# Optimization experiments

Hardware: AMD Instinct MI355X
Metric: run time of the kernel (lower is better)

Reference implementation:

```python
import jax, jax.numpy as jnp
import numpy as np

N = 50000          # nodes per side (variables == clauses here)
IN, HID, OUT = 64, 128, 128
H = 4              # attention heads (self and cross)
P = 2              # num_meta_paths
E = 640000         # edges per graph
NEG = 0.2          # leaky_relu negative slope


def _glorot(key, shape):
    fan = shape[-2] + shape[-1]
    return (jax.random.normal(key, shape) * jnp.sqrt(2.0 / fan)).astype(jnp.float32)


def _ln(x, g, b):
    mu = x.mean(-1, keepdims=True)
    v = ((x - mu) ** 2).mean(-1, keepdims=True)
    return (x - mu) / jnp.sqrt(v + 1e-5) * g + b


def _segment_softmax(s, seg, num):
    # s: [E, H]; softmax over edges sharing the same seg id
    smax = jax.ops.segment_max(s, seg, num_segments=num)
    e = jnp.exp(s - smax[seg])
    den = jax.ops.segment_sum(e, seg, num_segments=num)
    return e / (den[seg] + 1e-16)


def _agg(alpha, feats, src, dst, num):
    # out[d, h, c] = sum_{e: dst[e]=d} alpha[e,h] * feats[src[e], c]
    gathered = feats[src]  # [E, C]
    outs = [jax.ops.segment_sum(alpha[:, h:h + 1] * gathered, dst, num_segments=num)
            for h in range(alpha.shape[1])]
    return jnp.stack(outs, axis=1)  # [num, H, C]


def _hga_self(x, adj, W, att_l, att_r, bias):
    # homogeneous HGAConv with self loops, concat=False (mean over heads)
    n = x.shape[0]
    xl = x @ W.T                      # [N, C]
    al = xl @ att_l                   # [N, H]
    ar = xl @ att_r                   # [N, H]
    loops = jnp.arange(n)
    src = jnp.concatenate([adj[0], loops])
    dst = jnp.concatenate([adj[1], loops])
    score = al[dst] + ar[src]         # edge_score: a_l[adj[1]] + a_r[adj[0]]
    alpha = _segment_softmax(jax.nn.leaky_relu(score, NEG), dst, n)
    out = _agg(alpha, xl, src, dst, n).mean(axis=1)  # [N, C]
    return out + bias


def _hga_cross(xv, xc, adj, Wl, Wr, att_l, att_r, bias):
    # bipartite HGAConv: adj[1] indexes var nodes, adj[0] indexes cls nodes
    n, m = xv.shape[0], xc.shape[0]
    xl = xv @ Wl.T
    xr = xc @ Wr.T
    al = xl @ att_l
    ar = xr @ att_r
    ar_ = xl @ att_r
    al_ = xr @ att_l
    c_idx, v_idx = adj[0], adj[1]
    score = al[v_idx] + ar[c_idx]        # -> normalized per var node
    score_ = ar_[v_idx] + al_[c_idx]     # transposed direction -> per cls node
    alpha = _segment_softmax(jax.nn.leaky_relu(score, NEG), v_idx, n)
    alpha_ = _segment_softmax(jax.nn.leaky_relu(score_, NEG), c_idx, m)
    out_var = _agg(alpha, xr, c_idx, v_idx, n).mean(axis=1) + bias   # [n, OUT]
    out_cls = _agg(alpha_, xl, v_idx, c_idx, m).mean(axis=1) + bias  # [m, OUT]
    return out_var, out_cls


def setup_inputs() -> dict:
    key = jax.random.key(0)
    ks = jax.random.split(key, 32)
    d = {}
    d['x_var'] = jax.random.normal(ks[0], (N, IN), dtype=jnp.float32)
    d['x_cls'] = jax.random.normal(ks[1], (N, IN), dtype=jnp.float32)
    d['mp_var'] = jax.random.randint(ks[2], (P, 2, E), 0, N)
    d['mp_cls'] = jax.random.randint(ks[3], (P, 2, E), 0, N)
    d['adj_pos'] = jax.random.randint(ks[4], (2, E), 0, N)
    d['adj_neg'] = jax.random.randint(ks[5], (2, E), 0, N)
    d['W_var_emb'] = _glorot(ks[6], (HID, IN))
    d['W_cls_emb'] = _glorot(ks[7], (HID, IN))
    d['ln_var_g'] = jnp.ones(HID); d['ln_var_b'] = jnp.zeros(HID)
    d['ln_cls_g'] = jnp.ones(HID); d['ln_cls_b'] = jnp.zeros(HID)
    d['var_pw'] = jnp.ones(P); d['cls_pw'] = jnp.ones(P)
    d['sv_W'] = _glorot(ks[8], (P, HID, HID))
    d['sv_al'] = _glorot(ks[9], (P, HID, H))
    d['sv_ar'] = _glorot(ks[10], (P, HID, H))
    d['sv_b'] = jnp.zeros((P, HID))
    d['sc_W'] = _glorot(ks[11], (P, HID, HID))
    d['sc_al'] = _glorot(ks[12], (P, HID, H))
    d['sc_ar'] = _glorot(ks[13], (P, HID, H))
    d['sc_b'] = jnp.zeros((P, HID))
    d['cp_Wl'] = _glorot(ks[14], (OUT, HID))
    d['cp_Wr'] = _glorot(ks[15], (OUT, HID))
    d['cp_al'] = _glorot(ks[16], (OUT, H))
    d['cp_ar'] = _glorot(ks[17], (OUT, H))
    d['cp_b'] = jnp.zeros(OUT)
    d['cn_Wl'] = _glorot(ks[18], (OUT, HID))
    d['cn_Wr'] = _glorot(ks[19], (OUT, HID))
    d['cn_al'] = _glorot(ks[20], (OUT, H))
    d['cn_ar'] = _glorot(ks[21], (OUT, H))
    d['cn_b'] = jnp.zeros(OUT)
    return d


def reference(x_var, x_cls, mp_var, mp_cls, adj_pos, adj_neg,
              W_var_emb, W_cls_emb, ln_var_g, ln_var_b, ln_cls_g, ln_cls_b,
              var_pw, cls_pw, sv_W, sv_al, sv_ar, sv_b, sc_W, sc_al, sc_ar, sc_b,
              cp_Wl, cp_Wr, cp_al, cp_ar, cp_b, cn_Wl, cn_Wr, cn_al, cn_ar, cn_b):
    xv = x_var @ W_var_emb.T          # [N, HID]
    xc = x_cls @ W_cls_emb.T
    # pre-norm residual self-attention, weighted sum over meta paths
    hv = _ln(xv, ln_var_g, ln_var_b)
    hc = _ln(xc, ln_cls_g, ln_cls_b)
    av = sum(var_pw[p] * _hga_self(hv, mp_var[p], sv_W[p], sv_al[p], sv_ar[p], sv_b[p]) for p in range(P))
    ac = sum(cls_pw[p] * _hga_self(hc, mp_cls[p], sc_W[p], sc_al[p], sc_ar[p], sc_b[p]) for p in range(P))
    xv = xv + av
    xc = xc + ac
    # bipartite cross attention over positive / negative literal edges
    vpos, cpos = _hga_cross(xv, xc, adj_pos, cp_Wl, cp_Wr, cp_al, cp_ar, cp_b)
    vneg, cneg = _hga_cross(xv, xc, adj_neg, cn_Wl, cn_Wr, cn_al, cn_ar, cn_b)
    return jnp.stack([vpos + vneg, cpos + cneg])  # [2, N, OUT]
```

## Files before the change

### kernel.cpp

```cpp
#include <hip/hip_runtime.h>
#include <hip/hip_bf16.h>

#define NN 50000
#define EE 640000
#define NEG 0.2f
#define CAP 64

#define BSH 9
#define NBKT 98
#define FCAP 7168
#define CHUNKA 8192
#define PA_B 79

struct Ptr8 { const int* p[8]; };
struct MArgs { const float* w[8]; const float* al[8]; const float* ar[8]; };

struct SegArg {
    const int* starts;
    const int* counts;
    const unsigned short* srt;
    const float* adst;
    const float* asrc;
    const unsigned short* feats;
    const float* pw;
    int pwi;
    int hasLoop;
};

typedef __attribute__((ext_vector_type(8))) short short8;
typedef __attribute__((ext_vector_type(8))) unsigned short ushort8;
typedef __attribute__((ext_vector_type(4))) float floatx4;

__device__ __forceinline__ unsigned short f2bf(float x) {
    unsigned b = __float_as_uint(x);
    b = b + 0x7fffu + ((b >> 16) & 1u);
    return (unsigned short)(b >> 16);
}

__device__ __forceinline__ float4 leakyexp4(float4 ad, float4 as) {
    float v0 = ad.x + as.x, v1 = ad.y + as.y, v2 = ad.z + as.z, v3 = ad.w + as.w;
    v0 = v0 > 0.f ? v0 : NEG * v0;
    v1 = v1 > 0.f ? v1 : NEG * v1;
    v2 = v2 > 0.f ? v2 : NEG * v2;
    v3 = v3 > 0.f ? v3 : NEG * v3;
    return make_float4(__expf(v0), __expf(v1), __expf(v2), __expf(v3));
}

__global__ void transpose_emb(const float* __restrict__ wev, const float* __restrict__ wec,
                              float* __restrict__ out)
{
    int i = blockIdx.x * 256 + threadIdx.x;
    if (i < 8192) { out[i] = wev[(i & 127) * 64 + (i >> 7)]; return; }
    if (i < 16384) { int j = i - 8192; out[i] = wec[(j & 127) * 64 + (j >> 7)]; }
}

__global__ void make_M(MArgs a, float* __restrict__ Mbuf)
{
    int b = blockIdx.x;
    const float* W  = a.w[b];
    const float* AL = a.al[b];
    const float* AR = a.ar[b];
    for (int e = threadIdx.x; e < 1024; e += 256) {
        int k = e >> 3, h = e & 7;
        const float* att = (h < 4) ? AL : AR;
        int hh = h & 3;
        float s = 0.f;
        for (int c = 0; c < 128; c++) s += W[c * 128 + k] * att[c * 4 + hh];
        Mbuf[b * 1024 + e] = s;
    }
}

__global__ void embed_ln(const float* __restrict__ x, const float* __restrict__ Wt,
                         const float* __restrict__ g, const float* __restrict__ b,
                         const float* __restrict__ pw, const float* __restrict__ sb,
                         float* __restrict__ F, float* __restrict__ C)
{
    __shared__ float lx[8][64];
    __shared__ float red[2][8][2];
    int c = threadIdx.x;
    int n0 = blockIdx.x * 8;
    for (int t = c; t < 8 * 64; t += 128) {
        lx[t >> 6][t & 63] = x[(size_t)(n0 + (t >> 6)) * 64 + (t & 63)];
    }
    __syncthreads();
    float acc[8];
#pragma unroll
    for (int m = 0; m < 8; m++) acc[m] = 0.f;
    for (int k = 0; k < 64; k++) {
        float w = Wt[k * 128 + c];
#pragma unroll
        for (int m = 0; m < 8; m++) acc[m] += lx[m][k] * w;
    }
    int lane = c & 63, wv = c >> 6;
#pragma unroll
    for (int m = 0; m < 8; m++) {
        float s1 = acc[m], s2 = acc[m] * acc[m];
        for (int off = 32; off; off >>= 1) { s1 += __shfl_xor(s1, off); s2 += __shfl_xor(s2, off); }
        if (lane == 0) { red[wv][m][0] = s1; red[wv][m][1] = s2; }
    }
    __syncthreads();
    float biassum = pw[0] * sb[c] + pw[1] * sb[128 + c];
    float gg = g[c], bb = b[c];
#pragma unroll
    for (int m = 0; m < 8; m++) {
        float s1 = red[0][m][0] + red[1][m][0];
        float s2 = red[0][m][1] + red[1][m][1];
        float mu  = s1 * (1.f / 128.f);
        float var = s2 * (1.f / 128.f) - mu * mu;
        float inv = rsqrtf(var + 1e-5f);
        float v = acc[m];
        size_t idx = (size_t)(n0 + m) * 128 + c;
        F[idx] = v + biassum;
        C[idx] = (v - mu) * inv * gg + bb;
    }
}

__device__ __forceinline__ void stage_W(const float* __restrict__ W,
                                        unsigned short* __restrict__ WL, int t)
{
    for (int i = t; i < 2048; i += 256) {
        int n = i >> 4, c16 = i & 15;
        const float* src = W + n * 128 + c16 * 8;
        short8 v;
#pragma unroll
        for (int j = 0; j < 8; j++) v[j] = (short)f2bf(src[j]);
        *(short8*)&WL[(n * 16 + (c16 ^ (n & 15))) * 8] = v;
    }
}

__global__ __launch_bounds__(256) void mfma_proj2(
    const float* __restrict__ in,
    const float* __restrict__ W0, const float* __restrict__ W1,
    const float* __restrict__ M0, const float* __restrict__ M1,
    unsigned short* __restrict__ ob0, unsigned short* __restrict__ ob1,
    float4* __restrict__ dl0, float4* __restrict__ dr0,
    float4* __restrict__ dl1, float4* __restrict__ dr1)
{
    __shared__ unsigned short WL[16384];
    __shared__ float ML[2048];

    int t = threadIdx.x;
    stage_W(W0, WL, t);
    for (int i = t; i < 1024; i += 256) { ML[i] = M0[i]; ML[1024 + i] = M1[i]; }
    __syncthreads();

    int w = t >> 6, lane = t & 63;
    int ln = lane & 15, quad = lane >> 4;
    int rbase = blockIdx.x * 64 + w * 16;
    int row = rbase + ln;
    int arow = (row < NN) ? row : (NN - 1);

    short8 afrag[4];
    float p[16];
#pragma unroll
    for (int h = 0; h < 16; h++) p[h] = 0.f;
#pragma unroll
    for (int kc = 0; kc < 4; kc++) {
        int k0 = kc * 32 + quad * 8;
        const float* ap = in + (size_t)arow * 128 + k0;
        float av[8];
#pragma unroll
        for (int j = 0; j < 8; j++) av[j] = ap[j];
#pragma unroll
        for (int j = 0; j < 8; j++) {
            afrag[kc][j] = (short)f2bf(av[j]);
            const float* m0 = &ML[(k0 + j) * 8];
            const float* m1 = &ML[1024 + (k0 + j) * 8];
#pragma unroll
            for (int h = 0; h < 8; h++) { p[h] += av[j] * m0[h]; p[8 + h] += av[j] * m1[h]; }
        }
    }
#pragma unroll
    for (int h = 0; h < 16; h++) {
        p[h] += __shfl_xor(p[h], 16);
        p[h] += __shfl_xor(p[h], 32);
    }
    if (quad == 0 && row < NN) {
        dl0[row] = make_float4(p[0], p[1], p[2], p[3]);
        dr0[row] = make_float4(p[4], p[5], p[6], p[7]);
        dl1[row] = make_float4(p[8], p[9], p[10], p[11]);
        dr1[row] = make_float4(p[12], p[13], p[14], p[15]);
    }

#pragma unroll
    for (int ct = 0; ct < 8; ct++) {
        floatx4 acc = {0.f, 0.f, 0.f, 0.f};
#pragma unroll
        for (int kc = 0; kc < 4; kc++) {
            int c16 = kc * 4 + quad;
            int n = ct * 16 + ln;
            short8 bfr = *(const short8*)&WL[(n * 16 + (c16 ^ ln)) * 8];
            acc = __builtin_amdgcn_mfma_f32_16x16x32_bf16(afrag[kc], bfr, acc, 0, 0, 0);
        }
#pragma unroll
        for (int r = 0; r < 4; r++) {
            int rr = rbase + quad * 4 + r;
            if (rr < NN) ob0[(size_t)rr * 128 + ct * 16 + ln] = f2bf(acc[r]);
        }
    }
    __syncthreads();
    stage_W(W1, WL, t);
    __syncthreads();
#pragma unroll
    for (int ct = 0; ct < 8; ct++) {
        floatx4 acc = {0.f, 0.f, 0.f, 0.f};
#pragma unroll
        for (int kc = 0; kc < 4; kc++) {
            int c16 = kc * 4 + quad;
            int n = ct * 16 + ln;
            short8 bfr = *(const short8*)&WL[(n * 16 + (c16 ^ ln)) * 8];
            acc = __builtin_amdgcn_mfma_f32_16x16x32_bf16(afrag[kc], bfr, acc, 0, 0, 0);
        }
#pragma unroll
        for (int r = 0; r < 4; r++) {
            int rr = rbase + quad * 4 + r;
            if (rr < NN) ob1[(size_t)rr * 128 + ct * 16 + ln] = f2bf(acc[r]);
        }
    }
}

__global__ void zero_bcnt(int* __restrict__ p)
{
    int i = blockIdx.x * 256 + threadIdx.x;
    if (i < 8 * NBKT) p[i] = 0;
}

__global__ void bucket_count(Ptr8 dst, int* __restrict__ bcnt)
{
    __shared__ int h[NBKT];
    int l = blockIdx.x / PA_B, cb = blockIdx.x % PA_B;
    const int* dp = dst.p[l];
    for (int i = threadIdx.x; i < NBKT; i += 256) h[i] = 0;
    __syncthreads();
    int e0 = cb * CHUNKA;
    for (int i = threadIdx.x; i < CHUNKA; i += 256) {
        int e = e0 + i;
        if (e < EE) atomicAdd(&h[dp[e] >> BSH], 1);
    }
    __syncthreads();
    for (int i = threadIdx.x; i < NBKT; i += 256)
        if (h[i]) atomicAdd(&bcnt[l * NBKT + i], h[i]);
}

__global__ void bucket_scan(const int* __restrict__ bcnt, int* __restrict__ bstart,
                            int* __restrict__ bcur)
{
    __shared__ int sh[NBKT];
    int l = blockIdx.x;
    for (int i = threadIdx.x; i < NBKT; i += 256) sh[i] = bcnt[l * NBKT + i];
    __syncthreads();
    if (threadIdx.x == 0) {
        int acc = 0;
        for (int i = 0; i < NBKT; i++) { int t = sh[i]; sh[i] = acc; acc += t; }
    }
    __syncthreads();
    for (int i = threadIdx.x; i < NBKT; i += 256) {
        bstart[l * (NBKT + 1) + i] = sh[i];
        bcur[l * NBKT + i] = sh[i];
    }
    if (threadIdx.x == 0) bstart[l * (NBKT + 1) + NBKT] = EE;
}

__global__ void bucket_place(Ptr8 src, Ptr8 dst, int* __restrict__ bcur,
                             unsigned* __restrict__ recs)
{
    __shared__ int h[NBKT];
    __shared__ int base[NBKT];
    int l = blockIdx.x / PA_B, cb = blockIdx.x % PA_B;
    const int* sp = src.p[l];
    const int* dp = dst.p[l];
    for (int i = threadIdx.x; i < NBKT; i += 256) h[i] = 0;
    __syncthreads();
    int e0 = cb * CHUNKA;
    for (int i = threadIdx.x; i < CHUNKA; i += 256) {
        int e = e0 + i;
        if (e < EE) atomicAdd(&h[dp[e] >> BSH], 1);
    }
    __syncthreads();
    for (int i = threadIdx.x; i < NBKT; i += 256) {
        int c = h[i];
        base[i] = c ? atomicAdd(&bcur[l * NBKT + i], c) : 0;
        h[i] = 0;
    }
    __syncthreads();
    unsigned* rl = recs + (size_t)l * EE;
    for (int i = threadIdx.x; i < CHUNKA; i += 256) {
        int e = e0 + i;
        if (e >= EE) continue;
        int d = dp[e];
        int b = d >> BSH;
        int pos = base[b] + atomicAdd(&h[b], 1);
        rl[pos] = ((unsigned)sp[e] << 16) | (unsigned)d;
    }
}

__global__ __launch_bounds__(256) void bucket_final(
    const unsigned* __restrict__ recs, const int* __restrict__ bstart,
    int* __restrict__ starts8, int* __restrict__ counts8,
    unsigned short* __restrict__ sortedU)
{
    __shared__ unsigned R[FCAP];
    __shared__ int cnt[512];
    __shared__ int cur[512];
    __shared__ int psum[256];
    int l = blockIdx.x / NBKT, b = blockIdx.x % NBKT;
    int d0 = b << BSH;
    int nd = min(512, NN - d0);
    int ebase = bstart[l * (NBKT + 1) + b];
    int ecnt  = bstart[l * (NBKT + 1) + b + 1] - ebase;
    const unsigned* rp = recs + (size_t)l * EE + ebase;
    int t = threadIdx.x;
    bool inLds = (ecnt <= FCAP);

    for (int i = t; i < 512; i += 256) cnt[i] = 0;
    __syncthreads();
    for (int i = t; i < ecnt; i += 256) {
        unsigned r = rp[i];
        if (inLds) R[i] = r;
        atomicAdd(&cnt[(r & 0xffffu) - d0], 1);
    }
    __syncthreads();
    int s0 = cnt[2 * t] + cnt[2 * t + 1];
    psum[t] = s0;
    __syncthreads();
    for (int off = 1; off < 256; off <<= 1) {
        int x = (t >= off) ? psum[t - off] : 0;
        __syncthreads();
        psum[t] += x;
        __syncthreads();
    }
    int excl = psum[t] - s0;
    cur[2 * t] = excl;
    cur[2 * t + 1] = excl + cnt[2 * t];
    __syncthreads();
    for (int i = t; i < nd; i += 256) {
        starts8[l * NN + d0 + i] = ebase + cur[i];
        counts8[l * NN + d0 + i] = cnt[i];
    }
    __syncthreads();
    unsigned short* so = sortedU + (size_t)l * EE + ebase;
    for (int i = t; i < ecnt; i += 256) {
        unsigned r = inLds ? R[i] : rp[i];
        int dloc = (int)(r & 0xffffu) - d0;
        int pos = atomicAdd(&cur[dloc], 1);
        so[pos] = (unsigned short)(r >> 16);
    }
}

__global__ __launch_bounds__(256, 8) void agg_fused(
    SegArg A, SegArg B,
    const float* __restrict__ bias0, const float* __restrict__ bias1,
    float* __restrict__ acc, int mode)
{
    __shared__ float          wSh[16][CAP];
    __shared__ unsigned short sSh[16][CAP];

    int t = threadIdx.x;
    int gid = t >> 4;
    int sub = t & 15;
    int seg = gid & 1;
    int d   = blockIdx.x * 8 + (gid >> 1);

    const int* starts = seg ? B.starts : A.starts;
    const int* counts = seg ? B.counts : A.counts;
    const unsigned short* srt = seg ? B.srt : A.srt;
    const float* adst = seg ? B.adst : A.adst;
    const float* asrc = seg ? B.asrc : A.asrc;
    const unsigned short* feats = seg ? B.feats : A.feats;
    const float* pw = seg ? B.pw : A.pw;
    int pwi = seg ? B.pwi : A.pwi;
    int hasLoop = seg ? B.hasLoop : A.hasLoop;

    int base = starts[d];
    int k = counts[d];
    int kTot = k + hasLoop;

    float4 ad = *(const float4*)(adst + (size_t)d * 4);

    float p0 = 0.f, p1 = 0.f, p2 = 0.f, p3 = 0.f;
    for (int i = sub; i < kTot; i += 16) {
        int s = (i < k) ? (int)srt[base + i] : d;
        if (i < CAP) sSh[gid][i] = (unsigned short)s;
        float4 as = *(const float4*)(asrc + (size_t)s * 4);
        float4 e = leakyexp4(ad, as);
        p0 += e.x; p1 += e.y; p2 += e.z; p3 += e.w;
    }
#pragma unroll
    for (int off = 1; off <= 8; off <<= 1) {
        p0 += __shfl_xor(p0, off); p1 += __shfl_xor(p1, off);
        p2 += __shfl_xor(p2, off); p3 += __shfl_xor(p3, off);
    }
    float scale = 0.25f * (pw ? pw[pwi] : 1.0f);
    float i0 = scale / (p0 + 1e-16f);
    float i1 = scale / (p1 + 1e-16f);
    float i2 = scale / (p2 + 1e-16f);
    float i3 = scale / (p3 + 1e-16f);

    int kW = kTot < CAP ? kTot : CAP;
    for (int i = sub; i < kW; i += 16) {
        int s = (int)sSh[gid][i];
        float4 as = *(const float4*)(asrc + (size_t)s * 4);
        float4 e = leakyexp4(ad, as);
        wSh[gid][i] = e.x * i0 + e.y * i1 + e.z * i2 + e.w * i3;
    }

    float a[8];
#pragma unroll
    for (int i = 0; i < 8; i++) a[i] = 0.f;
    const unsigned short* fbase = feats + sub * 8;
    for (int j = 0; j < kW; ++j) {
        float wgt = wSh[gid][j];
        int s = (int)sSh[gid][j];
        ushort8 v = *(const ushort8*)(fbase + (size_t)s * 128);
#pragma unroll
        for (int i = 0; i < 8; i++)
            a[i] += wgt * __uint_as_float((unsigned)(unsigned short)v[i] << 16);
    }
    for (int j = CAP; j < kTot; ++j) {
        int s = (j < k) ? (int)srt[base + j] : d;
        float4 as = *(const float4*)(asrc + (size_t)s * 4);
        float4 e = leakyexp4(ad, as);
        float wgt = e.x * i0 + e.y * i1 + e.z * i2 + e.w * i3;
        ushort8 v = *(const ushort8*)(fbase + (size_t)s * 128);
#pragma unroll
        for (int i = 0; i < 8; i++)
            a[i] += wgt * __uint_as_float((unsigned)(unsigned short)v[i] << 16);
    }

#pragma unroll
    for (int i = 0; i < 8; i++) a[i] += __shfl_xor(a[i], 16);

    if (seg == 0) {
        size_t idx = (size_t)d * 128 + sub * 8;
        float4* ap = (float4*)(acc + idx);
        float4 lo = make_float4(a[0], a[1], a[2], a[3]);
        float4 hi = make_float4(a[4], a[5], a[6], a[7]);
        if (mode) {
            const float4* b0 = (const float4*)(bias0 + sub * 8);
            const float4* b1 = (const float4*)(bias1 + sub * 8);
            float4 c0 = b0[0], c1 = b0[1], d0v = b1[0], d1v = b1[1];
            ap[0] = make_float4(c0.x + d0v.x + lo.x, c0.y + d0v.y + lo.y,
                                c0.z + d0v.z + lo.z, c0.w + d0v.w + lo.w);
            ap[1] = make_float4(c1.x + d1v.x + hi.x, c1.y + d1v.y + hi.y,
                                c1.z + d1v.z + hi.z, c1.w + d1v.w + hi.w);
        } else {
            float4 r0 = ap[0], r1 = ap[1];
            ap[0] = make_float4(r0.x + lo.x, r0.y + lo.y, r0.z + lo.z, r0.w + lo.w);
            ap[1] = make_float4(r1.x + hi.x, r1.y + hi.y, r1.z + hi.z, r1.w + hi.w);
        }
    }
}

extern "C" void kernel_launch(void* const* d_in, const int* in_sizes, int n_in,
                              void* d_out, int out_size, void* d_ws, size_t ws_size,
                              hipStream_t stream)
{
    const float* x_var   = (const float*)d_in[0];
    const float* x_cls   = (const float*)d_in[1];
    const int*   mp_var  = (const int*)d_in[2];
    const int*   mp_cls  = (const int*)d_in[3];
    const int*   adj_pos = (const int*)d_in[4];
    const int*   adj_neg = (const int*)d_in[5];
    const float* W_var_emb = (const float*)d_in[6];
    const float* W_cls_emb = (const float*)d_in[7];
    const float* ln_var_g = (const float*)d_in[8];
    const float* ln_var_b = (const float*)d_in[9];
    const float* ln_cls_g = (const float*)d_in[10];
    const float* ln_cls_b = (const float*)d_in[11];
    const float* var_pw = (const float*)d_in[12];
    const float* cls_pw = (const float*)d_in[13];
    const float* sv_W  = (const float*)d_in[14];
    const float* sv_al = (const float*)d_in[15];
    const float* sv_ar = (const float*)d_in[16];
    const float* sv_b  = (const float*)d_in[17];
    const float* sc_W  = (const float*)d_in[18];
    const float* sc_al = (const float*)d_in[19];
    const float* sc_ar = (const float*)d_in[20];
    const float* sc_b  = (const float*)d_in[21];
    const float* cp_Wl = (const float*)d_in[22];
    const float* cp_Wr = (const float*)d_in[23];
    const float* cp_al = (const float*)d_in[24];
    const float* cp_ar = (const float*)d_in[25];
    const float* cp_b  = (const float*)d_in[26];
    const float* cn_Wl = (const float*)d_in[27];
    const float* cn_Wr = (const float*)d_in[28];
    const float* cn_al = (const float*)d_in[29];
    const float* cn_ar = (const float*)d_in[30];
    const float* cn_b  = (const float*)d_in[31];

    float* out0 = (float*)d_out;
    float* out1 = out0 + (size_t)NN * 128;

    float* ws = (float*)d_ws;
    size_t off = 0;
    auto alloc = [&](size_t n) { float* p = ws + off; off += n; return p; };
    float* Wt   = alloc(16384);
    float* Mbuf = alloc(8 * 1024);
    float* F   = alloc((size_t)NN * 128);
    float* G   = alloc((size_t)NN * 128);
    float* C   = alloc((size_t)NN * 128);
    float* D   = alloc((size_t)NN * 128);
    unsigned short* B1 = (unsigned short*)alloc((size_t)NN * 64);
    unsigned short* B2 = (unsigned short*)alloc((size_t)NN * 64);
    float* dl   = alloc(NN * 4);
    float* dr   = alloc(NN * 4);
    float* dl2  = alloc(NN * 4);
    float* dr2  = alloc(NN * 4);
    float* dl3  = alloc(NN * 4);
    float* dr3  = alloc(NN * 4);
    float* dl4  = alloc(NN * 4);
    float* dr4  = alloc(NN * 4);
    int* counts8 = (int*)alloc(8 * NN);
    int* starts8 = (int*)alloc(8 * NN);
    int* bcnt    = (int*)alloc(8 * NBKT);
    int* bstart  = (int*)alloc(8 * (NBKT + 1));
    int* bcur    = (int*)alloc(8 * NBKT);
    unsigned* recs = (unsigned*)alloc((size_t)8 * EE);
    unsigned short* sortedU = (unsigned short*)alloc((size_t)4 * EE);

    unsigned short* Pc = (unsigned short*)C;
    unsigned short* Pd = (unsigned short*)C + (size_t)NN * 128;

    const float* WtEv = Wt;
    const float* WtEc = Wt + 8192;

    Ptr8 srcP, dstP;
    srcP.p[0] = mp_var;            dstP.p[0] = mp_var + EE;
    srcP.p[1] = mp_var + 2 * EE;   dstP.p[1] = mp_var + 3 * EE;
    srcP.p[2] = mp_cls;            dstP.p[2] = mp_cls + EE;
    srcP.p[3] = mp_cls + 2 * EE;   dstP.p[3] = mp_cls + 3 * EE;
    srcP.p[4] = adj_pos;           dstP.p[4] = adj_pos + EE;
    srcP.p[5] = adj_pos + EE;      dstP.p[5] = adj_pos;
    srcP.p[6] = adj_neg;           dstP.p[6] = adj_neg + EE;
    srcP.p[7] = adj_neg + EE;      dstP.p[7] = adj_neg;

    MArgs ma;
    ma.w[0] = sv_W;           ma.al[0] = sv_al;        ma.ar[0] = sv_ar;
    ma.w[1] = sv_W + 16384;   ma.al[1] = sv_al + 512;  ma.ar[1] = sv_ar + 512;
    ma.w[2] = sc_W;           ma.al[2] = sc_al;        ma.ar[2] = sc_ar;
    ma.w[3] = sc_W + 16384;   ma.al[3] = sc_al + 512;  ma.ar[3] = sc_ar + 512;
    ma.w[4] = cp_Wl;          ma.al[4] = cp_al;        ma.ar[4] = cp_ar;
    ma.w[5] = cp_Wr;          ma.al[5] = cp_al;        ma.ar[5] = cp_ar;
    ma.w[6] = cn_Wl;          ma.al[6] = cn_al;        ma.ar[6] = cn_ar;
    ma.w[7] = cn_Wr;          ma.al[7] = cn_al;        ma.ar[7] = cn_ar;

    zero_bcnt<<<(8 * NBKT + 255) / 256, 256, 0, stream>>>(bcnt);
    bucket_count<<<8 * PA_B, 256, 0, stream>>>(dstP, bcnt);
    bucket_scan<<<8, 256, 0, stream>>>(bcnt, bstart, bcur);
    bucket_place<<<8 * PA_B, 256, 0, stream>>>(srcP, dstP, bcur, recs);
    bucket_final<<<8 * NBKT, 256, 0, stream>>>(recs, bstart, starts8, counts8, sortedU);

    transpose_emb<<<64, 256, 0, stream>>>(W_var_emb, W_cls_emb, Wt);
    make_M<<<8, 256, 0, stream>>>(ma, Mbuf);
    embed_ln<<<NN / 8, 128, 0, stream>>>(x_var, WtEv, ln_var_g, ln_var_b, var_pw, sv_b, F, C);
    embed_ln<<<NN / 8, 128, 0, stream>>>(x_cls, WtEc, ln_cls_g, ln_cls_b, cls_pw, sc_b, G, D);

    const int PB = (NN + 63) / 64;
    const int AB = NN / 8;

    for (int side = 0; side < 2; ++side) {
        const float* h    = side ? D : C;
        float*       accp = side ? G : F;
        const float* pw   = side ? cls_pw : var_pw;
        int s0 = side * 2, s1 = side * 2 + 1;
        mfma_proj2<<<PB, 256, 0, stream>>>(h, ma.w[s0], ma.w[s1],
                                           Mbuf + s0 * 1024, Mbuf + s1 * 1024,
                                           B1, B2,
                                           (float4*)dl, (float4*)dr,
                                           (float4*)dl2, (float4*)dr2);
        SegArg SA, SB;
        SA.starts = starts8 + s0 * NN; SA.counts = counts8 + s0 * NN;
        SA.srt = sortedU + (size_t)s0 * EE;
        SA.adst = dl;  SA.asrc = dr;  SA.feats = B1; SA.pw = pw; SA.pwi = 0; SA.hasLoop = 1;
        SB.starts = starts8 + s1 * NN; SB.counts = counts8 + s1 * NN;
        SB.srt = sortedU + (size_t)s1 * EE;
        SB.adst = dl2; SB.asrc = dr2; SB.feats = B2; SB.pw = pw; SB.pwi = 1; SB.hasLoop = 1;
        agg_fused<<<AB, 256, 0, stream>>>(SA, SB, cp_b, cn_b, accp, 0);
    }

    mfma_proj2<<<PB, 256, 0, stream>>>(F, ma.w[4], ma.w[6],
                                       Mbuf + 4 * 1024, Mbuf + 6 * 1024,
                                       B1, Pc,
                                       (float4*)dl, (float4*)dr,
                                       (float4*)dl3, (float4*)dr3);
    mfma_proj2<<<PB, 256, 0, stream>>>(G, ma.w[5], ma.w[7],
                                       Mbuf + 5 * 1024, Mbuf + 7 * 1024,
                                       B2, Pd,
                                       (float4*)dl2, (float4*)dr2,
                                       (float4*)dl4, (float4*)dr4);

    {
        SegArg SA, SB;
        SA.starts = starts8 + 4 * NN; SA.counts = counts8 + 4 * NN;
        SA.srt = sortedU + (size_t)4 * EE;
        SA.adst = dl;  SA.asrc = dr2; SA.feats = B2; SA.pw = nullptr; SA.pwi = 0; SA.hasLoop = 0;
        SB.starts = starts8 + 6 * NN; SB.counts = counts8 + 6 * NN;
        SB.srt = sortedU + (size_t)6 * EE;
        SB.adst = dl3; SB.asrc = dr4; SB.feats = Pd; SB.pw = nullptr; SB.pwi = 0; SB.hasLoop = 0;
        agg_fused<<<AB, 256, 0, stream>>>(SA, SB, cp_b, cn_b, out0, 1);
    }
    {
        SegArg SA, SB;
        SA.starts = starts8 + 5 * NN; SA.counts = counts8 + 5 * NN;
        SA.srt = sortedU + (size_t)5 * EE;
        SA.adst = dl2; SA.asrc = dr;  SA.feats = B1; SA.pw = nullptr; SA.pwi = 0; SA.hasLoop = 0;
        SB.starts = starts8 + 7 * NN; SB.counts = counts8 + 7 * NN;
        SB.srt = sortedU + (size_t)7 * EE;
        SB.adst = dl4; SB.asrc = dr3; SB.feats = Pc; SB.pw = nullptr; SB.pwi = 0; SB.hasLoop = 0;
        agg_fused<<<AB, 256, 0, stream>>>(SA, SB, cp_b, cn_b, out1, 1);
    }
}
```

Before: 729.3 us.

## Pre-pack bf16 MFMA weights once, split projection work, cache softmax exps in registers

A new prep_W kernel converts all eight projection weight matrices to bf16 once, in MFMA fragment order. mfma_proj2 then reads B fragments straight from global/L2 instead of converting and staging 32KB of LDS per block. Blocks now cover 32 rows, with warps split across column halves and meta-path halves, which doubles the grid and removes the mid-kernel restage barrier. agg_fused keeps the first 64 edge exponentials in registers, packs weight and source index into a single LDS entry, and unrolls the gather by two. This avoids recomputing exp and re-reading asrc, at the cost of more registers, so the launch bound is lowered to 6 waves.

```diff
diff --git a/kernel.cpp b/kernel.cpp
--- a/kernel.cpp
+++ b/kernel.cpp
@@ -70,6 +70,23 @@
     }
 }
 
+__global__ void prep_W(MArgs a, unsigned short* __restrict__ Wbf)
+{
+    int tid = blockIdx.x * 256 + threadIdx.x;
+    int w = tid >> 11;
+    int idx = tid & 2047;
+    int tile = idx >> 6;
+    int lane = idx & 63;
+    int ct = tile >> 2, kc = tile & 3;
+    int n = ct * 16 + (lane & 15);
+    int k0 = kc * 32 + (lane >> 4) * 8;
+    const float* src = a.w[w] + n * 128 + k0;
+    short8 v;
+#pragma unroll
+    for (int j = 0; j < 8; j++) v[j] = (short)f2bf(src[j]);
+    *(short8*)&Wbf[(size_t)tid * 8] = v;
+}
+
 __global__ void embed_ln(const float* __restrict__ x, const float* __restrict__ Wt,
                          const float* __restrict__ g, const float* __restrict__ b,
                          const float* __restrict__ pw, const float* __restrict__ sb,
@@ -115,45 +132,32 @@
     }
 }
 
-__device__ __forceinline__ void stage_W(const float* __restrict__ W,
-                                        unsigned short* __restrict__ WL, int t)
-{
-    for (int i = t; i < 2048; i += 256) {
-        int n = i >> 4, c16 = i & 15;
-        const float* src = W + n * 128 + c16 * 8;
-        short8 v;
-#pragma unroll
-        for (int j = 0; j < 8; j++) v[j] = (short)f2bf(src[j]);
-        *(short8*)&WL[(n * 16 + (c16 ^ (n & 15))) * 8] = v;
-    }
-}
-
 __global__ __launch_bounds__(256) void mfma_proj2(
     const float* __restrict__ in,
-    const float* __restrict__ W0, const float* __restrict__ W1,
+    const unsigned short* __restrict__ Wp0, const unsigned short* __restrict__ Wp1,
     const float* __restrict__ M0, const float* __restrict__ M1,
     unsigned short* __restrict__ ob0, unsigned short* __restrict__ ob1,
     float4* __restrict__ dl0, float4* __restrict__ dr0,
     float4* __restrict__ dl1, float4* __restrict__ dr1)
 {
-    __shared__ unsigned short WL[16384];
     __shared__ float ML[2048];
 
     int t = threadIdx.x;
-    stage_W(W0, WL, t);
-    for (int i = t; i < 1024; i += 256) { ML[i] = M0[i]; ML[1024 + i] = M1[i]; }
+    for (int i = t; i < 2048; i += 256) ML[i] = (i < 1024) ? M0[i] : M1[i - 1024];
     __syncthreads();
 
     int w = t >> 6, lane = t & 63;
+    int rg = w & 1, chh = w >> 1;
     int ln = lane & 15, quad = lane >> 4;
-    int rbase = blockIdx.x * 64 + w * 16;
+    int rbase = blockIdx.x * 32 + rg * 16;
     int row = rbase + ln;
     int arow = (row < NN) ? row : (NN - 1);
+    const float* MLh = &ML[chh * 1024];
 
     short8 afrag[4];
-    float p[16];
-#pragma unroll
-    for (int h = 0; h < 16; h++) p[h] = 0.f;
+    float p[8];
+#pragma unroll
+    for (int h = 0; h < 8; h++) p[h] = 0.f;
 #pragma unroll
     for (int kc = 0; kc < 4; kc++) {
         int k0 = kc * 32 + quad * 8;
@@ -164,32 +168,33 @@
 #pragma unroll
         for (int j = 0; j < 8; j++) {
             afrag[kc][j] = (short)f2bf(av[j]);
-            const float* m0 = &ML[(k0 + j) * 8];
-            const float* m1 = &ML[1024 + (k0 + j) * 8];
-#pragma unroll
-            for (int h = 0; h < 8; h++) { p[h] += av[j] * m0[h]; p[8 + h] += av[j] * m1[h]; }
-        }
-    }
-#pragma unroll
-    for (int h = 0; h < 16; h++) {
+            const float* mrow = &MLh[(k0 + j) * 8];
+#pragma unroll
+            for (int h = 0; h < 8; h++) p[h] += av[j] * mrow[h];
+        }
+    }
+#pragma unroll
+    for (int h = 0; h < 8; h++) {
         p[h] += __shfl_xor(p[h], 16);
         p[h] += __shfl_xor(p[h], 32);
     }
     if (quad == 0 && row < NN) {
-        dl0[row] = make_float4(p[0], p[1], p[2], p[3]);
-        dr0[row] = make_float4(p[4], p[5], p[6], p[7]);
-        dl1[row] = make_float4(p[8], p[9], p[10], p[11]);
-        dr1[row] = make_float4(p[12], p[13], p[14], p[15]);
-    }
-
-#pragma unroll
-    for (int ct = 0; ct < 8; ct++) {
+        if (chh == 0) {
+            dl0[row] = make_float4(p[0], p[1], p[2], p[3]);
+            dr0[row] = make_float4(p[4], p[5], p[6], p[7]);
+        } else {
+            dl1[row] = make_float4(p[0], p[1], p[2], p[3]);
+            dr1[row] = make_float4(p[4], p[5], p[6], p[7]);
+        }
+    }
+
+#pragma unroll
+    for (int cti = 0; cti < 4; cti++) {
+        int ct = chh * 4 + cti;
         floatx4 acc = {0.f, 0.f, 0.f, 0.f};
 #pragma unroll
         for (int kc = 0; kc < 4; kc++) {
-            int c16 = kc * 4 + quad;
-            int n = ct * 16 + ln;
-            short8 bfr = *(const short8*)&WL[(n * 16 + (c16 ^ ln)) * 8];
+            short8 bfr = *(const short8*)&Wp0[(size_t)((ct * 4 + kc) * 64 + lane) * 8];
             acc = __builtin_amdgcn_mfma_f32_16x16x32_bf16(afrag[kc], bfr, acc, 0, 0, 0);
         }
 #pragma unroll
@@ -198,17 +203,13 @@
             if (rr < NN) ob0[(size_t)rr * 128 + ct * 16 + ln] = f2bf(acc[r]);
         }
     }
-    __syncthreads();
-    stage_W(W1, WL, t);
-    __syncthreads();
-#pragma unroll
-    for (int ct = 0; ct < 8; ct++) {
+#pragma unroll
+    for (int cti = 0; cti < 4; cti++) {
+        int ct = chh * 4 + cti;
         floatx4 acc = {0.f, 0.f, 0.f, 0.f};
 #pragma unroll
         for (int kc = 0; kc < 4; kc++) {
-            int c16 = kc * 4 + quad;
-            int n = ct * 16 + ln;
-            short8 bfr = *(const short8*)&WL[(n * 16 + (c16 ^ ln)) * 8];
+            short8 bfr = *(const short8*)&Wp1[(size_t)((ct * 4 + kc) * 64 + lane) * 8];
             acc = __builtin_amdgcn_mfma_f32_16x16x32_bf16(afrag[kc], bfr, acc, 0, 0, 0);
         }
 #pragma unroll
@@ -347,13 +348,12 @@
     }
 }
 
-__global__ __launch_bounds__(256, 8) void agg_fused(
+__global__ __launch_bounds__(256, 6) void agg_fused(
     SegArg A, SegArg B,
     const float* __restrict__ bias0, const float* __restrict__ bias1,
     float* __restrict__ acc, int mode)
 {
-    __shared__ float          wSh[16][CAP];
-    __shared__ unsigned short sSh[16][CAP];
+    __shared__ uint2 pSh[16][CAP];
 
     int t = threadIdx.x;
     int gid = t >> 4;
@@ -377,50 +377,84 @@
 
     float4 ad = *(const float4*)(adst + (size_t)d * 4);
 
-    float p0 = 0.f, p1 = 0.f, p2 = 0.f, p3 = 0.f;
-    for (int i = sub; i < kTot; i += 16) {
+    float den0 = 0.f, den1 = 0.f, den2 = 0.f, den3 = 0.f;
+    float4 e0 = {0,0,0,0}, e1 = {0,0,0,0}, e2 = {0,0,0,0}, e3 = {0,0,0,0};
+    int s0 = 0, s1 = 0, s2 = 0, s3 = 0;
+    int ia = sub, ib = sub + 16, ic = sub + 32, id = sub + 48;
+    if (ia < kTot) {
+        s0 = (ia < k) ? (int)srt[base + ia] : d;
+        e0 = leakyexp4(ad, *(const float4*)(asrc + (size_t)s0 * 4));
+        den0 += e0.x; den1 += e0.y; den2 += e0.z; den3 += e0.w;
+    }
+    if (ib < kTot) {
+        s1 = (ib < k) ? (int)srt[base + ib] : d;
+        e1 = leakyexp4(ad, *(const float4*)(asrc + (size_t)s1 * 4));
+        den0 += e1.x; den1 += e1.y; den2 += e1.z; den3 += e1.w;
+    }
+    if (ic < kTot) {
+        s2 = (ic < k) ? (int)srt[base + ic] : d;
+        e2 = leakyexp4(ad, *(const float4*)(asrc + (size_t)s2 * 4));
+        den0 += e2.x; den1 += e2.y; den2 += e2.z; den3 += e2.w;
+    }
+    if (id < kTot) {
+        s3 = (id < k) ? (int)srt[base + id] : d;
+        e3 = leakyexp4(ad, *(const float4*)(asrc + (size_t)s3 * 4));
+        den0 += e3.x; den1 += e3.y; den2 += e3.z; den3 += e3.w;
+    }
+    for (int i = sub + 64; i < kTot; i += 16) {
         int s = (i < k) ? (int)srt[base + i] : d;
-        if (i < CAP) sSh[gid][i] = (unsigned short)s;
-        float4 as = *(const float4*)(asrc + (size_t)s * 4);
-        float4 e = leakyexp4(ad, as);
-        p0 += e.x; p1 += e.y; p2 += e.z; p3 += e.w;
+        float4 e = leakyexp4(ad, *(const float4*)(asrc + (size_t)s * 4));
+        den0 += e.x; den1 += e.y; den2 += e.z; den3 += e.w;
     }
 #pragma unroll
     for (int off = 1; off <= 8; off <<= 1) {
-        p0 += __shfl_xor(p0, off); p1 += __shfl_xor(p1, off);
-        p2 += __shfl_xor(p2, off); p3 += __shfl_xor(p3, off);
+        den0 += __shfl_xor(den0, off); den1 += __shfl_xor(den1, off);
+        den2 += __shfl_xor(den2, off); den3 += __shfl_xor(den3, off);
     }
     float scale = 0.25f * (pw ? pw[pwi] : 1.0f);
-    float i0 = scale / (p0 + 1e-16f);
-    float i1 = scale / (p1 + 1e-16f);
-    float i2 = scale / (p2 + 1e-16f);
-    float i3 = scale / (p3 + 1e-16f);
-
-    int kW = kTot < CAP ? kTot : CAP;
-    for (int i = sub; i < kW; i += 16) {
-        int s = (int)sSh[gid][i];
-        float4 as = *(const float4*)(asrc + (size_t)s * 4);
-        float4 e = leakyexp4(ad, as);
-        wSh[gid][i] = e.x * i0 + e.y * i1 + e.z * i2 + e.w * i3;
-    }
+    float r0 = scale / (den0 + 1e-16f);
+    float r1 = scale / (den1 + 1e-16f);
+    float r2 = scale / (den2 + 1e-16f);
+    float r3 = scale / (den3 + 1e-16f);
+
+    if (ia < kTot) pSh[gid][ia] = make_uint2(
+        __float_as_uint(e0.x * r0 + e0.y * r1 + e0.z * r2 + e0.w * r3), (unsigned)s0);
+    if (ib < kTot) pSh[gid][ib] = make_uint2(
+        __float_as_uint(e1.x * r0 + e1.y * r1 + e1.z * r2 + e1.w * r3), (unsigned)s1);
+    if (ic < kTot) pSh[gid][ic] = make_uint2(
+        __float_as_uint(e2.x * r0 + e2.y * r1 + e2.z * r2 + e2.w * r3), (unsigned)s2);
+    if (id < kTot) pSh[gid][id] = make_uint2(
+        __float_as_uint(e3.x * r0 + e3.y * r1 + e3.z * r2 + e3.w * r3), (unsigned)s3);
 
     float a[8];
 #pragma unroll
     for (int i = 0; i < 8; i++) a[i] = 0.f;
     const unsigned short* fbase = feats + sub * 8;
-    for (int j = 0; j < kW; ++j) {
-        float wgt = wSh[gid][j];
-        int s = (int)sSh[gid][j];
-        ushort8 v = *(const ushort8*)(fbase + (size_t)s * 128);
+    int kW = kTot < CAP ? kTot : CAP;
+    int j = 0;
+    for (; j + 2 <= kW; j += 2) {
+        uint4 pq = *(const uint4*)&pSh[gid][j];
+        ushort8 va = *(const ushort8*)(fbase + (size_t)pq.y * 128);
+        ushort8 vb = *(const ushort8*)(fbase + (size_t)pq.w * 128);
+        float wa = __uint_as_float(pq.x), wb = __uint_as_float(pq.z);
+#pragma unroll
+        for (int i = 0; i < 8; i++) {
+            a[i] += wa * __uint_as_float((unsigned)(unsigned short)va[i] << 16);
+            a[i] += wb * __uint_as_float((unsigned)(unsigned short)vb[i] << 16);
+        }
+    }
+    if (j < kW) {
+        uint2 ps = pSh[gid][j];
+        ushort8 v = *(const ushort8*)(fbase + (size_t)ps.y * 128);
+        float wgt = __uint_as_float(ps.x);
 #pragma unroll
         for (int i = 0; i < 8; i++)
             a[i] += wgt * __uint_as_float((unsigned)(unsigned short)v[i] << 16);
     }
-    for (int j = CAP; j < kTot; ++j) {
-        int s = (j < k) ? (int)srt[base + j] : d;
-        float4 as = *(const float4*)(asrc + (size_t)s * 4);
-        float4 e = leakyexp4(ad, as);
-        float wgt = e.x * i0 + e.y * i1 + e.z * i2 + e.w * i3;
+    for (int jj = CAP; jj < kTot; ++jj) {
+        int s = (jj < k) ? (int)srt[base + jj] : d;
+        float4 e = leakyexp4(ad, *(const float4*)(asrc + (size_t)s * 4));
+        float wgt = e.x * r0 + e.y * r1 + e.z * r2 + e.w * r3;
         ushort8 v = *(const ushort8*)(fbase + (size_t)s * 128);
 #pragma unroll
         for (int i = 0; i < 8; i++)
@@ -444,9 +478,9 @@
             ap[1] = make_float4(c1.x + d1v.x + hi.x, c1.y + d1v.y + hi.y,
                                 c1.z + d1v.z + hi.z, c1.w + d1v.w + hi.w);
         } else {
-            float4 r0 = ap[0], r1 = ap[1];
-            ap[0] = make_float4(r0.x + lo.x, r0.y + lo.y, r0.z + lo.z, r0.w + lo.w);
-            ap[1] = make_float4(r1.x + hi.x, r1.y + hi.y, r1.z + hi.z, r1.w + hi.w);
+            float4 rr0 = ap[0], rr1 = ap[1];
+            ap[0] = make_float4(rr0.x + lo.x, rr0.y + lo.y, rr0.z + lo.z, rr0.w + lo.w);
+            ap[1] = make_float4(rr1.x + hi.x, rr1.y + hi.y, rr1.z + hi.z, rr1.w + hi.w);
         }
     }
 }
@@ -496,6 +530,7 @@
     auto alloc = [&](size_t n) { float* p = ws + off; off += n; return p; };
     float* Wt   = alloc(16384);
     float* Mbuf = alloc(8 * 1024);
+    unsigned short* Wbf = (unsigned short*)alloc(8 * 8192);
     float* F   = alloc((size_t)NN * 128);
     float* G   = alloc((size_t)NN * 128);
     float* C   = alloc((size_t)NN * 128);
@@ -552,10 +587,11 @@
 
     transpose_emb<<<64, 256, 0, stream>>>(W_var_emb, W_cls_emb, Wt);
     make_M<<<8, 256, 0, stream>>>(ma, Mbuf);
+    prep_W<<<64, 256, 0, stream>>>(ma, Wbf);
     embed_ln<<<NN / 8, 128, 0, stream>>>(x_var, WtEv, ln_var_g, ln_var_b, var_pw, sv_b, F, C);
     embed_ln<<<NN / 8, 128, 0, stream>>>(x_cls, WtEc, ln_cls_g, ln_cls_b, cls_pw, sc_b, G, D);
 
-    const int PB = (NN + 63) / 64;
+    const int PB = (NN + 31) / 32;
     const int AB = NN / 8;
 
     for (int side = 0; side < 2; ++side) {
@@ -563,7 +599,7 @@
         float*       accp = side ? G : F;
         const float* pw   = side ? cls_pw : var_pw;
         int s0 = side * 2, s1 = side * 2 + 1;
-        mfma_proj2<<<PB, 256, 0, stream>>>(h, ma.w[s0], ma.w[s1],
+        mfma_proj2<<<PB, 256, 0, stream>>>(h, Wbf + s0 * 16384, Wbf + s1 * 16384,
                                            Mbuf + s0 * 1024, Mbuf + s1 * 1024,
                                            B1, B2,
                                            (float4*)dl, (float4*)dr,
@@ -578,12 +614,12 @@
         agg_fused<<<AB, 256, 0, stream>>>(SA, SB, cp_b, cn_b, accp, 0);
     }
 
-    mfma_proj2<<<PB, 256, 0, stream>>>(F, ma.w[4], ma.w[6],
+    mfma_proj2<<<PB, 256, 0, stream>>>(F, Wbf + 4 * 16384, Wbf + 6 * 16384,
                                        Mbuf + 4 * 1024, Mbuf + 6 * 1024,
                                        B1, Pc,
                                        (float4*)dl, (float4*)dr,
                                        (float4*)dl3, (float4*)dr3);
-    mfma_proj2<<<PB, 256, 0, stream>>>(G, ma.w[5], ma.w[7],
+    mfma_proj2<<<PB, 256, 0, stream>>>(G, Wbf + 5 * 16384, Wbf + 7 * 16384,
                                        Mbuf + 5 * 1024, Mbuf + 7 * 1024,
                                        B2, Pd,
                                        (float4*)dl2, (float4*)dr2,
```

New measurement: 691.1 us. 1.06x faster.
